# Kernel optimization log

Measured on AMD Instinct MI355X. Metric: run time of the kernel, lower is better.

## Reference

```python
import jax, jax.numpy as jnp
import numpy as np

CANVAS = 28
MARGIN = 2
HALF = CANVAS / 2.0          # 14
SCALE = CANVAS / 2.0 - MARGIN  # 12
P = 2        # num_paths
SEG = 4      # final segments
T = 8        # curve samples per bezier segment
AA = 2       # 2x2 = 4 anti-alias subsamples per pixel


def _lin(x, w, b):
    return x @ w + b


def _render(cp, widths, alphas):
    """diffvg-style rasterizer.
    cp: [B,P,S,4,2] cubic bezier control points, widths/alphas: [B,P].
    Returns [B,1,H,W] image over white background (paths paint dark).
    """
    B = cp.shape[0]
    t = jnp.linspace(0.0, 1.0, T)
    mt = 1.0 - t
    basis = jnp.stack([mt**3, 3*mt**2*t, 3*mt*t**2, t**3], axis=1)  # [T,4]
    pts = jnp.einsum('tk,bpskd->bpstd', basis, cp)                   # [B,P,S,T,2]
    q = pts.reshape(B, P, SEG * T, 2)                                # polyline [B,P,M,2]

    # 2x2 subpixel sample grid over the canvas
    Nf = CANVAS * AA
    c = (jnp.arange(Nf, dtype=jnp.float32) + 0.5) / AA               # fine coords
    sy, sx = jnp.meshgrid(c, c, indexing='ij')
    s = jnp.stack([sx.ravel(), sy.ravel()], axis=-1)                 # [Ns,2] (x,y)

    # stroke coverage: distance from each sample to nearest curve sample
    qq = jnp.sum(q * q, axis=-1)                                     # [B,P,M]
    ss = jnp.sum(s * s, axis=-1)                                     # [Ns]
    cr = jnp.einsum('bpmd,nd->bpmn', q, s)                           # [B,P,M,Ns]
    d2 = jnp.maximum(qq[..., None] + ss - 2.0 * cr, 0.0)
    dist = jnp.sqrt(jnp.min(d2, axis=2))                             # [B,P,Ns]
    stroke = jnp.clip(widths[..., None] * 0.5 + 0.5 - dist, 0.0, 1.0)

    # fill coverage: even-odd crossing number on the closed polyline
    qn = jnp.roll(q, -1, axis=2)
    x0, y0 = q[..., 0], q[..., 1]
    x1, y1 = qn[..., 0], qn[..., 1]
    syf, sxf = s[:, 1], s[:, 0]
    crossing_band = (y0[..., None] > syf) != (y1[..., None] > syf)   # [B,P,M,Ns]
    te = (syf - y0[..., None]) / (y1[..., None] - y0[..., None] + 1e-8)
    xint = x0[..., None] + te * (x1 - x0)[..., None]
    ncross = jnp.sum((crossing_band & (sxf < xint)).astype(jnp.int32), axis=2)
    inside = (ncross % 2).astype(dist.dtype)                         # [B,P,Ns]

    cov = jnp.maximum(inside, stroke)
    img = jnp.prod(1.0 - alphas[..., None] * cov, axis=1)            # composite over paths, bg=1
    img = img.reshape(B, CANVAS, AA, CANVAS, AA).mean(axis=(2, 4))   # AA resolve
    return img[:, None]                                              # [B,1,H,W]


def setup_inputs() -> dict:
    key = jax.random.key(0)
    ks = jax.random.split(key, 16)
    def W(k, i, o):
        return jax.random.normal(k, (i, o), jnp.float32) / np.sqrt(i).astype(np.float32)
    B = 128
    return {
        'x': jax.random.uniform(ks[0], (B, 1, 28, 28), jnp.float32),
        'eps': jax.random.normal(ks[1], (B, 64), jnp.float32),
        'enc_w1': W(ks[2], 784, 256), 'enc_b1': jnp.zeros((256,), jnp.float32),
        'enc_w2': W(ks[3], 256, 256), 'enc_b2': jnp.zeros((256,), jnp.float32),
        'mu_w': W(ks[4], 256, 64), 'mu_b': jnp.zeros((64,), jnp.float32),
        'lv_w': W(ks[5], 256, 64), 'lv_b': jnp.zeros((64,), jnp.float32),
        'dec_w1': W(ks[6], 64, 512), 'dec_b1': jnp.zeros((512,), jnp.float32),
        'dec_w2': W(ks[7], 512, 512), 'dec_b2': jnp.zeros((512,), jnp.float32),
        'cp_w': W(ks[8], 512, 28), 'cp_b': jnp.zeros((28,), jnp.float32),
        'ref_w1': W(ks[9], 92, 512), 'ref_b1': jnp.zeros((512,), jnp.float32),
        'ref_w2': W(ks[10], 512, 52), 'ref_b2': jnp.zeros((52,), jnp.float32),
        'wd_w': W(ks[11], 512, 2), 'wd_b': jnp.zeros((2,), jnp.float32),
        'al_w': W(ks[12], 512, 2), 'al_b': jnp.zeros((2,), jnp.float32),
    }


def reference(x, eps, enc_w1, enc_b1, enc_w2, enc_b2, mu_w, mu_b, lv_w, lv_b,
              dec_w1, dec_b1, dec_w2, dec_b2, cp_w, cp_b,
              ref_w1, ref_b1, ref_w2, ref_b2, wd_w, wd_b, al_w, al_b):
    B = x.shape[0]
    # encoder
    h = jax.nn.leaky_relu(_lin(x.reshape(B, -1), enc_w1, enc_b1), 0.2)
    h = jax.nn.leaky_relu(_lin(h, enc_w2, enc_b2), 0.2)
    mu = _lin(h, mu_w, mu_b)
    logvar = _lin(h, lv_w, lv_b)
    z = mu + eps * jnp.exp(0.5 * logvar)
    # hierarchical decoder
    h2 = jax.nn.selu(_lin(jax.nn.selu(_lin(z, dec_w1, dec_b1)), dec_w2, dec_b2))
    coarse = jnp.tanh(_lin(h2, cp_w, cp_b)).reshape(B, P, 7, 2) * SCALE + HALF
    pts_norm = (coarse - HALF) / SCALE
    h_in = jnp.concatenate([z, pts_norm.reshape(B, -1)], axis=-1)
    refined = jnp.tanh(_lin(jax.nn.selu(_lin(h_in, ref_w1, ref_b1)), ref_w2, ref_b2))
    points = refined.reshape(B, P, 13, 2) * SCALE + HALF
    seg_idx = 3 * jnp.arange(SEG)[:, None] + jnp.arange(4)[None, :]  # [S,4]
    control_points = points[:, :, seg_idx, :]                         # [B,P,S,4,2]
    widths = jax.nn.sigmoid(_lin(h2, wd_w, wd_b)) * 2.0 + 1.0
    alphas = jax.nn.sigmoid(_lin(h2, al_w, al_b))
    rendered = 1.0 - _render(control_points, widths, alphas)          # white digit on black
    return (rendered, mu, logvar, control_points, widths, alphas)
```

## Files before the change

### kernel.cpp

```cpp
#include <hip/hip_runtime.h>
#include <math.h>


#define O_MU  100352
#define O_LV  108544
#define O_CP  116736
#define O_WD  124928
#define O_AL  125184

#define W_H1   0
#define W_HE   32768
#define W_MUT  65536
#define W_LVT  73728
#define W_D1   81920
#define W_H2   147456
#define W_PN   212992
#define W_R1   216576
#define W_PT   282112
#define W_WA   288768

__device__ __forceinline__ float leaky(float x) { return x >= 0.f ? x : 0.2f * x; }
__device__ __forceinline__ float seluf(float x) {
    const float s = 1.0507009873554805f, a = 1.6732632423543772f;
    return x > 0.f ? s * x : s * (a * expm1f(x));
}
__device__ __forceinline__ float sigm(float x) { return 1.f / (1.f + expf(-x)); }

__global__ __launch_bounds__(512)
void enc1_k(const float* __restrict__ x, const float* __restrict__ w,
            const float* __restrict__ b, float* __restrict__ outT) {
    __shared__ float part[8][64];
    const int j = blockIdx.x >> 1, h = blockIdx.x & 1;
    const int tid = threadIdx.x, lane = tid & 63, ks = tid >> 6;
    const int r = h * 64 + lane;
    const float* __restrict__ xr = x + r * 784;
    float acc = 0.f;
    const int k0 = ks * 98;
#pragma unroll 7
    for (int i = 0; i < 98; i++)
        acc = fmaf(xr[k0 + i], w[(k0 + i) * 256 + j], acc);
    part[ks][lane] = acc;
    __syncthreads();
    if (tid < 64) {
        float s = b[j];
#pragma unroll
        for (int q = 0; q < 8; q++) s += part[q][tid];
        outT[j * 128 + h * 64 + tid] = leaky(s);
    }
}

__global__ __launch_bounds__(512)
void enc2_k(const float* __restrict__ inT, const float* __restrict__ w,
            const float* __restrict__ b, float* __restrict__ outT) {
    __shared__ float part[8][64];
    const int j = blockIdx.x >> 1, h = blockIdx.x & 1;
    const int tid = threadIdx.x, lane = tid & 63, ks = tid >> 6;
    const int r = h * 64 + lane;
    float acc = 0.f;
    const int k0 = ks * 32;
#pragma unroll 8
    for (int i = 0; i < 32; i++)
        acc = fmaf(inT[(k0 + i) * 128 + r], w[(k0 + i) * 256 + j], acc);
    part[ks][lane] = acc;
    __syncthreads();
    if (tid < 64) {
        float s = b[j];
#pragma unroll
        for (int q = 0; q < 8; q++) s += part[q][tid];
        outT[j * 128 + h * 64 + tid] = leaky(s);
    }
}

__global__ __launch_bounds__(512)
void mulv_k(const float* __restrict__ heT,
            const float* __restrict__ mu_w, const float* __restrict__ mu_b,
            const float* __restrict__ lv_w, const float* __restrict__ lv_b,
            float* __restrict__ muT, float* __restrict__ lvT,
            float* __restrict__ out) {
    __shared__ float part[8][64];
    const int meta = blockIdx.x >> 1, h = blockIdx.x & 1;
    const int head = meta >> 6, col = meta & 63;
    const float* __restrict__ w = head ? lv_w : mu_w;
    const int tid = threadIdx.x, lane = tid & 63, ks = tid >> 6;
    const int r = h * 64 + lane;
    float acc = 0.f;
    const int k0 = ks * 32;
#pragma unroll 8
    for (int i = 0; i < 32; i++)
        acc = fmaf(heT[(k0 + i) * 128 + r], w[(k0 + i) * 64 + col], acc);
    part[ks][lane] = acc;
    __syncthreads();
    if (tid < 64) {
        float s = (head ? lv_b : mu_b)[col];
#pragma unroll
        for (int q = 0; q < 8; q++) s += part[q][tid];
        const int rr = h * 64 + tid;
        (head ? lvT : muT)[col * 128 + rr] = s;
        out[(head ? O_LV : O_MU) + rr * 64 + col] = s;
    }
}

__global__ __launch_bounds__(512)
void dec1_k(const float* __restrict__ muT, const float* __restrict__ lvT,
            const float* __restrict__ eps, const float* __restrict__ w,
            const float* __restrict__ b, float* __restrict__ outT) {
    __shared__ float part[8][2][64];
    const int j0 = (blockIdx.x >> 1) * 2, h = blockIdx.x & 1;
    const int tid = threadIdx.x, lane = tid & 63, ks = tid >> 6;
    const int r = h * 64 + lane;
    float a0 = 0.f, a1 = 0.f;
    const int k0 = ks * 8;
#pragma unroll
    for (int i = 0; i < 8; i++) {
        const int k = k0 + i;
        float zv = fmaf(eps[r * 64 + k], expf(0.5f * lvT[k * 128 + r]), muT[k * 128 + r]);
        a0 = fmaf(zv, w[k * 512 + j0],     a0);
        a1 = fmaf(zv, w[k * 512 + j0 + 1], a1);
    }
    part[ks][0][lane] = a0; part[ks][1][lane] = a1;
    __syncthreads();
    if (tid < 128) {
        const int c = tid >> 6, ll = tid & 63;
        float s = b[j0 + c];
#pragma unroll
        for (int q = 0; q < 8; q++) s += part[q][c][ll];
        outT[(j0 + c) * 128 + h * 64 + ll] = seluf(s);
    }
}

__global__ __launch_bounds__(512)
void dec2_k(const float* __restrict__ inT, const float* __restrict__ w,
            const float* __restrict__ b, float* __restrict__ outT) {
    __shared__ float part[8][2][64];
    const int j0 = (blockIdx.x >> 1) * 2, h = blockIdx.x & 1;
    const int tid = threadIdx.x, lane = tid & 63, ks = tid >> 6;
    const int r = h * 64 + lane;
    float a0 = 0.f, a1 = 0.f;
    const int k0 = ks * 64;
#pragma unroll 4
    for (int i = 0; i < 64; i++) {
        const float v = inT[(k0 + i) * 128 + r];
        a0 = fmaf(v, w[(k0 + i) * 512 + j0],     a0);
        a1 = fmaf(v, w[(k0 + i) * 512 + j0 + 1], a1);
    }
    part[ks][0][lane] = a0; part[ks][1][lane] = a1;
    __syncthreads();
    if (tid < 128) {
        const int c = tid >> 6, ll = tid & 63;
        float s = b[j0 + c];
#pragma unroll
        for (int q = 0; q < 8; q++) s += part[q][c][ll];
        outT[(j0 + c) * 128 + h * 64 + ll] = seluf(s);
    }
}

__global__ __launch_bounds__(512)
void heads_k(const float* __restrict__ h2T,
             const float* __restrict__ cp_w, const float* __restrict__ cp_b,
             const float* __restrict__ wd_w, const float* __restrict__ wd_b,
             const float* __restrict__ al_w, const float* __restrict__ al_b,
             float* __restrict__ pnT, float* __restrict__ waT,
             float* __restrict__ out) {
    __shared__ float part[8][64];
    const int j = blockIdx.x >> 1, h = blockIdx.x & 1;
    const float* __restrict__ w; int ldw, col;
    if (j < 28)      { w = cp_w; ldw = 28; col = j; }
    else if (j < 30) { w = wd_w; ldw = 2;  col = j - 28; }
    else             { w = al_w; ldw = 2;  col = j - 30; }
    const int tid = threadIdx.x, lane = tid & 63, ks = tid >> 6;
    const int r = h * 64 + lane;
    float acc = 0.f;
    const int k0 = ks * 64;
#pragma unroll 8
    for (int i = 0; i < 64; i++)
        acc = fmaf(h2T[(k0 + i) * 128 + r], w[(k0 + i) * ldw + col], acc);
    part[ks][lane] = acc;
    __syncthreads();
    if (tid < 64) {
        float s = 0.f;
#pragma unroll
        for (int q = 0; q < 8; q++) s += part[q][tid];
        const int rr = h * 64 + tid;
        if (j < 28) {
            pnT[j * 128 + rr] = tanhf(s + cp_b[col]);
        } else if (j < 30) {
            float v = fmaf(sigm(s + wd_b[col]), 2.f, 1.f);
            out[O_WD + rr * 2 + col] = v; waT[col * 128 + rr] = v;
        } else {
            float v = sigm(s + al_b[col]);
            out[O_AL + rr * 2 + col] = v; waT[(2 + col) * 128 + rr] = v;
        }
    }
}

__global__ __launch_bounds__(512)
void ref1_k(const float* __restrict__ muT, const float* __restrict__ lvT,
            const float* __restrict__ eps, const float* __restrict__ pnT,
            const float* __restrict__ w, const float* __restrict__ b,
            float* __restrict__ outT) {
    __shared__ float part[8][2][64];
    const int j0 = (blockIdx.x >> 1) * 2, h = blockIdx.x & 1;
    const int tid = threadIdx.x, lane = tid & 63, ks = tid >> 6;
    const int r = h * 64 + lane;
    float a0 = 0.f, a1 = 0.f;
#pragma unroll
    for (int i = 0; i < 12; i++) {
        const int k = ks * 12 + i;
        if (k < 92) {
            float v = (k < 64)
                ? fmaf(eps[r * 64 + k], expf(0.5f * lvT[k * 128 + r]), muT[k * 128 + r])
                : pnT[(k - 64) * 128 + r];
            a0 = fmaf(v, w[k * 512 + j0],     a0);
            a1 = fmaf(v, w[k * 512 + j0 + 1], a1);
        }
    }
    part[ks][0][lane] = a0; part[ks][1][lane] = a1;
    __syncthreads();
    if (tid < 128) {
        const int c = tid >> 6, ll = tid & 63;
        float s = b[j0 + c];
#pragma unroll
        for (int q = 0; q < 8; q++) s += part[q][c][ll];
        outT[(j0 + c) * 128 + h * 64 + ll] = seluf(s);
    }
}

__global__ __launch_bounds__(512)
void ref2_k(const float* __restrict__ r1T, const float* __restrict__ w,
            const float* __restrict__ b, float* __restrict__ PT) {
    __shared__ float part[8][64];
    const int j = blockIdx.x >> 1, h = blockIdx.x & 1;
    const int tid = threadIdx.x, lane = tid & 63, ks = tid >> 6;
    const int r = h * 64 + lane;
    float acc = 0.f;
    const int k0 = ks * 64;
#pragma unroll 8
    for (int i = 0; i < 64; i++)
        acc = fmaf(r1T[(k0 + i) * 128 + r], w[(k0 + i) * 52 + j], acc);
    part[ks][lane] = acc;
    __syncthreads();
    if (tid < 64) {
        float s = b[j];
#pragma unroll
        for (int q = 0; q < 8; q++) s += part[q][tid];
        PT[j * 128 + h * 64 + tid] = fmaf(tanhf(s), 12.f, 14.f);
    }
}

__global__ __launch_bounds__(512)
void raster_k(const float* __restrict__ PT, const float* __restrict__ waT,
              float* __restrict__ out) {
    __shared__ float sP[56];
    __shared__ float sWA[4];
    __shared__ float sQ[128];
    const int bid = blockIdx.x;
    const int row = bid / 7, chunk = bid - row * 7;
    const int tid = threadIdx.x;
    if (tid < 52) sP[tid] = PT[tid * 128 + row];
    if (tid >= 64 && tid < 68) sWA[tid - 64] = waT[(tid - 64) * 128 + row];
    __syncthreads();
    if (chunk == 0 && tid < 64) {
        const int idx = tid, p = idx >> 5, rest = idx & 31;
        const int s = rest >> 3, kk = (rest >> 1) & 3, d = idx & 1;
        out[O_CP + row * 64 + idx] = sP[p * 26 + (3 * s + kk) * 2 + d];
    }
    if (tid < 128) {
        const int idx = tid, p = idx >> 6, s = (idx >> 4) & 3, ti = (idx >> 1) & 7, d = idx & 1;
        const float t = (float)ti / 7.0f, mt = 1.0f - t;
        const float c0 = mt * mt * mt, c1 = 3.f * mt * mt * t;
        const float c2 = 3.f * mt * t * t, c3 = t * t * t;
        const float* base = sP + p * 26 + 6 * s + d;
        sQ[idx] = c0 * base[0] + c1 * base[2] + c2 * base[4] + c3 * base[6];
    }
    __syncthreads();
    if (tid < 448) {
        const int pixel = chunk * 112 + (tid >> 2), sub = tid & 3;
        const int py = pixel / 28, px = pixel - py * 28;
        const float sy = ((float)(2 * py + (sub >> 1)) + 0.5f) * 0.5f;
        const float sx = ((float)(2 * px + (sub & 1)) + 0.5f) * 0.5f;
        const float2* __restrict__ sQ2 = (const float2*)sQ;
        float img = 1.0f;
#pragma unroll
        for (int p = 0; p < 2; p++) {
            float dmin2 = 1e30f;
            int cnt = 0;
            float2 cur = sQ2[p * 32];
            bool bp = cur.y > sy;
#pragma unroll
            for (int m = 0; m < 32; m++) {
                float2 nxt = sQ2[p * 32 + ((m + 1) & 31)];
                float dx = sx - cur.x;
                float dy = sy - cur.y;
                dmin2 = fminf(dmin2, fmaf(dx, dx, dy * dy));
                bool bn = nxt.y > sy;
                float den = nxt.y - cur.y + 1e-8f;
                float lhs = dx * den;
                float rhs = dy * (nxt.x - cur.x);
                if ((bp != bn) && ((lhs < rhs) == (den > 0.0f))) cnt++;
                cur = nxt;
                bp = bn;
            }
            float dist = sqrtf(dmin2);
            float stroke = fminf(fmaxf(fmaf(sWA[p], 0.5f, 0.5f) - dist, 0.f), 1.f);
            float cov = fmaxf((float)(cnt & 1), stroke);
            img *= fmaf(-sWA[2 + p], cov, 1.0f);
        }
        img += __shfl_xor(img, 1);
        img += __shfl_xor(img, 2);
        if (sub == 0) out[row * 784 + pixel] = 1.0f - 0.25f * img;
    }
}

extern "C" void kernel_launch(void* const* d_in, const int* in_sizes, int n_in,
                              void* d_out, int out_size, void* d_ws, size_t ws_size,
                              hipStream_t stream) {
    const float* x      = (const float*)d_in[0];
    const float* eps    = (const float*)d_in[1];
    const float* enc_w1 = (const float*)d_in[2];
    const float* enc_b1 = (const float*)d_in[3];
    const float* enc_w2 = (const float*)d_in[4];
    const float* enc_b2 = (const float*)d_in[5];
    const float* mu_w   = (const float*)d_in[6];
    const float* mu_b   = (const float*)d_in[7];
    const float* lv_w   = (const float*)d_in[8];
    const float* lv_b   = (const float*)d_in[9];
    const float* dec_w1 = (const float*)d_in[10];
    const float* dec_b1 = (const float*)d_in[11];
    const float* dec_w2 = (const float*)d_in[12];
    const float* dec_b2 = (const float*)d_in[13];
    const float* cp_w   = (const float*)d_in[14];
    const float* cp_b   = (const float*)d_in[15];
    const float* ref_w1 = (const float*)d_in[16];
    const float* ref_b1 = (const float*)d_in[17];
    const float* ref_w2 = (const float*)d_in[18];
    const float* ref_b2 = (const float*)d_in[19];
    const float* wd_w   = (const float*)d_in[20];
    const float* wd_b   = (const float*)d_in[21];
    const float* al_w   = (const float*)d_in[22];
    const float* al_b   = (const float*)d_in[23];

    float* out = (float*)d_out;
    float* ws  = (float*)d_ws;

    enc1_k <<<512, 512, 0, stream>>>(x, enc_w1, enc_b1, ws + W_H1);
    enc2_k <<<512, 512, 0, stream>>>(ws + W_H1, enc_w2, enc_b2, ws + W_HE);
    mulv_k <<<256, 512, 0, stream>>>(ws + W_HE, mu_w, mu_b, lv_w, lv_b,
                                     ws + W_MUT, ws + W_LVT, out);
    dec1_k <<<512, 512, 0, stream>>>(ws + W_MUT, ws + W_LVT, eps,
                                     dec_w1, dec_b1, ws + W_D1);
    dec2_k <<<512, 512, 0, stream>>>(ws + W_D1, dec_w2, dec_b2, ws + W_H2);
    heads_k<<<64, 512, 0, stream>>>(ws + W_H2, cp_w, cp_b, wd_w, wd_b, al_w, al_b,
                                    ws + W_PN, ws + W_WA, out);
    ref1_k <<<512, 512, 0, stream>>>(ws + W_MUT, ws + W_LVT, eps, ws + W_PN,
                                     ref_w1, ref_b1, ws + W_R1);
    ref2_k <<<104, 512, 0, stream>>>(ws + W_R1, ref_w2, ref_b2, ws + W_PT);
    raster_k<<<896, 512, 0, stream>>>(ws + W_PT, ws + W_WA, out);
}
```

Measured before the change: 190.0 us.

## Fuse all nine stages into one persistent kernel with grid barriers

Replaces nine separate kernel launches with a single persistent kernel of 256 blocks. Stages are separated by atomic-counter grid barriers in a zeroed workspace. Blocks loop over work items where the old grids were larger. This removes per-launch overhead and inter-kernel gaps, but adds a memset launch and relies on all 256 blocks being co-resident. The spin barrier has a timeout that could break silently, and its relaxed atomics plus a compiler-only fence may not guarantee cross-block memory visibility.

```diff
diff --git a/kernel.cpp b/kernel.cpp
--- a/kernel.cpp
+++ b/kernel.cpp
@@ -18,6 +18,8 @@
 #define W_R1   216576
 #define W_PT   282112
 #define W_WA   288768
+#define W_BAR  289280
+#define NBLK   256
 
 __device__ __forceinline__ float leaky(float x) { return x >= 0.f ? x : 0.2f * x; }
 __device__ __forceinline__ float seluf(float x) {
@@ -26,288 +28,315 @@
 }
 __device__ __forceinline__ float sigm(float x) { return 1.f / (1.f + expf(-x)); }
 
+__device__ __forceinline__ void stws(float* p, float v) {
+    __hip_atomic_store(p, v, __ATOMIC_RELAXED, __HIP_MEMORY_SCOPE_AGENT);
+}
+
+__device__ __forceinline__ void arrive_wait(unsigned* c) {
+    __syncthreads();
+    if (threadIdx.x == 0) {
+        __hip_atomic_fetch_add(c, 1u, __ATOMIC_RELAXED, __HIP_MEMORY_SCOPE_AGENT);
+        unsigned tries = 0;
+        while (__hip_atomic_load(c, __ATOMIC_RELAXED, __HIP_MEMORY_SCOPE_AGENT) < NBLK) {
+            __builtin_amdgcn_s_sleep(4);
+            if (++tries > (1u << 16)) break;
+        }
+    }
+    __syncthreads();
+    asm volatile("" ::: "memory");
+}
+
 __global__ __launch_bounds__(512)
-void enc1_k(const float* __restrict__ x, const float* __restrict__ w,
-            const float* __restrict__ b, float* __restrict__ outT) {
-    __shared__ float part[8][64];
-    const int j = blockIdx.x >> 1, h = blockIdx.x & 1;
-    const int tid = threadIdx.x, lane = tid & 63, ks = tid >> 6;
-    const int r = h * 64 + lane;
-    const float* __restrict__ xr = x + r * 784;
-    float acc = 0.f;
-    const int k0 = ks * 98;
-#pragma unroll 7
-    for (int i = 0; i < 98; i++)
-        acc = fmaf(xr[k0 + i], w[(k0 + i) * 256 + j], acc);
-    part[ks][lane] = acc;
-    __syncthreads();
-    if (tid < 64) {
-        float s = b[j];
-#pragma unroll
-        for (int q = 0; q < 8; q++) s += part[q][tid];
-        outT[j * 128 + h * 64 + tid] = leaky(s);
-    }
-}
-
-__global__ __launch_bounds__(512)
-void enc2_k(const float* __restrict__ inT, const float* __restrict__ w,
-            const float* __restrict__ b, float* __restrict__ outT) {
-    __shared__ float part[8][64];
-    const int j = blockIdx.x >> 1, h = blockIdx.x & 1;
-    const int tid = threadIdx.x, lane = tid & 63, ks = tid >> 6;
-    const int r = h * 64 + lane;
-    float acc = 0.f;
-    const int k0 = ks * 32;
-#pragma unroll 8
-    for (int i = 0; i < 32; i++)
-        acc = fmaf(inT[(k0 + i) * 128 + r], w[(k0 + i) * 256 + j], acc);
-    part[ks][lane] = acc;
-    __syncthreads();
-    if (tid < 64) {
-        float s = b[j];
-#pragma unroll
-        for (int q = 0; q < 8; q++) s += part[q][tid];
-        outT[j * 128 + h * 64 + tid] = leaky(s);
-    }
-}
-
-__global__ __launch_bounds__(512)
-void mulv_k(const float* __restrict__ heT,
-            const float* __restrict__ mu_w, const float* __restrict__ mu_b,
-            const float* __restrict__ lv_w, const float* __restrict__ lv_b,
-            float* __restrict__ muT, float* __restrict__ lvT,
-            float* __restrict__ out) {
-    __shared__ float part[8][64];
-    const int meta = blockIdx.x >> 1, h = blockIdx.x & 1;
-    const int head = meta >> 6, col = meta & 63;
-    const float* __restrict__ w = head ? lv_w : mu_w;
-    const int tid = threadIdx.x, lane = tid & 63, ks = tid >> 6;
-    const int r = h * 64 + lane;
-    float acc = 0.f;
-    const int k0 = ks * 32;
-#pragma unroll 8
-    for (int i = 0; i < 32; i++)
-        acc = fmaf(heT[(k0 + i) * 128 + r], w[(k0 + i) * 64 + col], acc);
-    part[ks][lane] = acc;
-    __syncthreads();
-    if (tid < 64) {
-        float s = (head ? lv_b : mu_b)[col];
-#pragma unroll
-        for (int q = 0; q < 8; q++) s += part[q][tid];
-        const int rr = h * 64 + tid;
-        (head ? lvT : muT)[col * 128 + rr] = s;
-        out[(head ? O_LV : O_MU) + rr * 64 + col] = s;
-    }
-}
-
-__global__ __launch_bounds__(512)
-void dec1_k(const float* __restrict__ muT, const float* __restrict__ lvT,
-            const float* __restrict__ eps, const float* __restrict__ w,
-            const float* __restrict__ b, float* __restrict__ outT) {
-    __shared__ float part[8][2][64];
-    const int j0 = (blockIdx.x >> 1) * 2, h = blockIdx.x & 1;
-    const int tid = threadIdx.x, lane = tid & 63, ks = tid >> 6;
-    const int r = h * 64 + lane;
-    float a0 = 0.f, a1 = 0.f;
-    const int k0 = ks * 8;
-#pragma unroll
-    for (int i = 0; i < 8; i++) {
-        const int k = k0 + i;
-        float zv = fmaf(eps[r * 64 + k], expf(0.5f * lvT[k * 128 + r]), muT[k * 128 + r]);
-        a0 = fmaf(zv, w[k * 512 + j0],     a0);
-        a1 = fmaf(zv, w[k * 512 + j0 + 1], a1);
-    }
-    part[ks][0][lane] = a0; part[ks][1][lane] = a1;
-    __syncthreads();
-    if (tid < 128) {
-        const int c = tid >> 6, ll = tid & 63;
-        float s = b[j0 + c];
-#pragma unroll
-        for (int q = 0; q < 8; q++) s += part[q][c][ll];
-        outT[(j0 + c) * 128 + h * 64 + ll] = seluf(s);
-    }
-}
-
-__global__ __launch_bounds__(512)
-void dec2_k(const float* __restrict__ inT, const float* __restrict__ w,
-            const float* __restrict__ b, float* __restrict__ outT) {
-    __shared__ float part[8][2][64];
-    const int j0 = (blockIdx.x >> 1) * 2, h = blockIdx.x & 1;
-    const int tid = threadIdx.x, lane = tid & 63, ks = tid >> 6;
-    const int r = h * 64 + lane;
-    float a0 = 0.f, a1 = 0.f;
-    const int k0 = ks * 64;
-#pragma unroll 4
-    for (int i = 0; i < 64; i++) {
-        const float v = inT[(k0 + i) * 128 + r];
-        a0 = fmaf(v, w[(k0 + i) * 512 + j0],     a0);
-        a1 = fmaf(v, w[(k0 + i) * 512 + j0 + 1], a1);
-    }
-    part[ks][0][lane] = a0; part[ks][1][lane] = a1;
-    __syncthreads();
-    if (tid < 128) {
-        const int c = tid >> 6, ll = tid & 63;
-        float s = b[j0 + c];
-#pragma unroll
-        for (int q = 0; q < 8; q++) s += part[q][c][ll];
-        outT[(j0 + c) * 128 + h * 64 + ll] = seluf(s);
-    }
-}
-
-__global__ __launch_bounds__(512)
-void heads_k(const float* __restrict__ h2T,
-             const float* __restrict__ cp_w, const float* __restrict__ cp_b,
-             const float* __restrict__ wd_w, const float* __restrict__ wd_b,
-             const float* __restrict__ al_w, const float* __restrict__ al_b,
-             float* __restrict__ pnT, float* __restrict__ waT,
-             float* __restrict__ out) {
-    __shared__ float part[8][64];
-    const int j = blockIdx.x >> 1, h = blockIdx.x & 1;
-    const float* __restrict__ w; int ldw, col;
-    if (j < 28)      { w = cp_w; ldw = 28; col = j; }
-    else if (j < 30) { w = wd_w; ldw = 2;  col = j - 28; }
-    else             { w = al_w; ldw = 2;  col = j - 30; }
-    const int tid = threadIdx.x, lane = tid & 63, ks = tid >> 6;
-    const int r = h * 64 + lane;
-    float acc = 0.f;
-    const int k0 = ks * 64;
-#pragma unroll 8
-    for (int i = 0; i < 64; i++)
-        acc = fmaf(h2T[(k0 + i) * 128 + r], w[(k0 + i) * ldw + col], acc);
-    part[ks][lane] = acc;
-    __syncthreads();
-    if (tid < 64) {
-        float s = 0.f;
-#pragma unroll
-        for (int q = 0; q < 8; q++) s += part[q][tid];
-        const int rr = h * 64 + tid;
-        if (j < 28) {
-            pnT[j * 128 + rr] = tanhf(s + cp_b[col]);
-        } else if (j < 30) {
-            float v = fmaf(sigm(s + wd_b[col]), 2.f, 1.f);
-            out[O_WD + rr * 2 + col] = v; waT[col * 128 + rr] = v;
-        } else {
-            float v = sigm(s + al_b[col]);
-            out[O_AL + rr * 2 + col] = v; waT[(2 + col) * 128 + rr] = v;
-        }
-    }
-}
-
-__global__ __launch_bounds__(512)
-void ref1_k(const float* __restrict__ muT, const float* __restrict__ lvT,
-            const float* __restrict__ eps, const float* __restrict__ pnT,
-            const float* __restrict__ w, const float* __restrict__ b,
-            float* __restrict__ outT) {
-    __shared__ float part[8][2][64];
-    const int j0 = (blockIdx.x >> 1) * 2, h = blockIdx.x & 1;
-    const int tid = threadIdx.x, lane = tid & 63, ks = tid >> 6;
-    const int r = h * 64 + lane;
-    float a0 = 0.f, a1 = 0.f;
-#pragma unroll
-    for (int i = 0; i < 12; i++) {
-        const int k = ks * 12 + i;
-        if (k < 92) {
-            float v = (k < 64)
-                ? fmaf(eps[r * 64 + k], expf(0.5f * lvT[k * 128 + r]), muT[k * 128 + r])
-                : pnT[(k - 64) * 128 + r];
-            a0 = fmaf(v, w[k * 512 + j0],     a0);
-            a1 = fmaf(v, w[k * 512 + j0 + 1], a1);
-        }
-    }
-    part[ks][0][lane] = a0; part[ks][1][lane] = a1;
-    __syncthreads();
-    if (tid < 128) {
-        const int c = tid >> 6, ll = tid & 63;
-        float s = b[j0 + c];
-#pragma unroll
-        for (int q = 0; q < 8; q++) s += part[q][c][ll];
-        outT[(j0 + c) * 128 + h * 64 + ll] = seluf(s);
-    }
-}
-
-__global__ __launch_bounds__(512)
-void ref2_k(const float* __restrict__ r1T, const float* __restrict__ w,
-            const float* __restrict__ b, float* __restrict__ PT) {
-    __shared__ float part[8][64];
-    const int j = blockIdx.x >> 1, h = blockIdx.x & 1;
-    const int tid = threadIdx.x, lane = tid & 63, ks = tid >> 6;
-    const int r = h * 64 + lane;
-    float acc = 0.f;
-    const int k0 = ks * 64;
-#pragma unroll 8
-    for (int i = 0; i < 64; i++)
-        acc = fmaf(r1T[(k0 + i) * 128 + r], w[(k0 + i) * 52 + j], acc);
-    part[ks][lane] = acc;
-    __syncthreads();
-    if (tid < 64) {
-        float s = b[j];
-#pragma unroll
-        for (int q = 0; q < 8; q++) s += part[q][tid];
-        PT[j * 128 + h * 64 + tid] = fmaf(tanhf(s), 12.f, 14.f);
-    }
-}
-
-__global__ __launch_bounds__(512)
-void raster_k(const float* __restrict__ PT, const float* __restrict__ waT,
-              float* __restrict__ out) {
+void vae_flow(const float* __restrict__ x, const float* __restrict__ eps,
+              const float* __restrict__ enc_w1, const float* __restrict__ enc_b1,
+              const float* __restrict__ enc_w2, const float* __restrict__ enc_b2,
+              const float* __restrict__ mu_w, const float* __restrict__ mu_b,
+              const float* __restrict__ lv_w, const float* __restrict__ lv_b,
+              const float* __restrict__ dec_w1, const float* __restrict__ dec_b1,
+              const float* __restrict__ dec_w2, const float* __restrict__ dec_b2,
+              const float* __restrict__ cp_w, const float* __restrict__ cp_b,
+              const float* __restrict__ ref_w1, const float* __restrict__ ref_b1,
+              const float* __restrict__ ref_w2, const float* __restrict__ ref_b2,
+              const float* __restrict__ wd_w, const float* __restrict__ wd_b,
+              const float* __restrict__ al_w, const float* __restrict__ al_b,
+              float* __restrict__ out, float* __restrict__ ws) {
+    __shared__ float sPart[1024];
     __shared__ float sP[56];
     __shared__ float sWA[4];
     __shared__ float sQ[128];
-    const int bid = blockIdx.x;
-    const int row = bid / 7, chunk = bid - row * 7;
+
+    const int b = blockIdx.x;
     const int tid = threadIdx.x;
-    if (tid < 52) sP[tid] = PT[tid * 128 + row];
-    if (tid >= 64 && tid < 68) sWA[tid - 64] = waT[(tid - 64) * 128 + row];
-    __syncthreads();
-    if (chunk == 0 && tid < 64) {
-        const int idx = tid, p = idx >> 5, rest = idx & 31;
-        const int s = rest >> 3, kk = (rest >> 1) & 3, d = idx & 1;
-        out[O_CP + row * 64 + idx] = sP[p * 26 + (3 * s + kk) * 2 + d];
-    }
-    if (tid < 128) {
-        const int idx = tid, p = idx >> 6, s = (idx >> 4) & 3, ti = (idx >> 1) & 7, d = idx & 1;
-        const float t = (float)ti / 7.0f, mt = 1.0f - t;
-        const float c0 = mt * mt * mt, c1 = 3.f * mt * mt * t;
-        const float c2 = 3.f * mt * t * t, c3 = t * t * t;
-        const float* base = sP + p * 26 + 6 * s + d;
-        sQ[idx] = c0 * base[0] + c1 * base[2] + c2 * base[4] + c3 * base[6];
-    }
-    __syncthreads();
-    if (tid < 448) {
-        const int pixel = chunk * 112 + (tid >> 2), sub = tid & 3;
-        const int py = pixel / 28, px = pixel - py * 28;
-        const float sy = ((float)(2 * py + (sub >> 1)) + 0.5f) * 0.5f;
-        const float sx = ((float)(2 * px + (sub & 1)) + 0.5f) * 0.5f;
+    const int lane = tid & 63, ks = tid >> 6;
+
+    float* const h1T = ws + W_H1;
+    float* const heT = ws + W_HE;
+    float* const muT = ws + W_MUT;
+    float* const lvT = ws + W_LVT;
+    float* const d1T = ws + W_D1;
+    float* const h2T = ws + W_H2;
+    float* const pnT = ws + W_PN;
+    float* const r1T = ws + W_R1;
+    float* const PT  = ws + W_PT;
+    float* const waT = ws + W_WA;
+    unsigned* const bar = (unsigned*)(ws + W_BAR);
+
+    for (int cc = 0; cc < 2; ++cc) {
+        const int c = b + cc * 256;
+        const int j = c >> 1, h = c & 1;
+        const int r = h * 64 + lane;
+        const float* __restrict__ xr = x + r * 784;
+        const int k0 = ks * 98;
+        float acc = 0.f;
+#pragma unroll 7
+        for (int i = 0; i < 98; i++)
+            acc = fmaf(xr[k0 + i], enc_w1[(k0 + i) * 256 + j], acc);
+        sPart[ks * 64 + lane] = acc;
+        __syncthreads();
+        if (tid < 64) {
+            float s = enc_b1[j];
+#pragma unroll
+            for (int q = 0; q < 8; q++) s += sPart[q * 64 + tid];
+            stws(h1T + j * 128 + h * 64 + tid, leaky(s));
+        }
+        __syncthreads();
+    }
+    arrive_wait(bar + 0);
+
+    for (int cc = 0; cc < 2; ++cc) {
+        const int c = b + cc * 256;
+        const int j = c >> 1, h = c & 1;
+        const int r = h * 64 + lane;
+        const int k0 = ks * 32;
+        float acc = 0.f;
+#pragma unroll 8
+        for (int i = 0; i < 32; i++)
+            acc = fmaf(h1T[(k0 + i) * 128 + r], enc_w2[(k0 + i) * 256 + j], acc);
+        sPart[ks * 64 + lane] = acc;
+        __syncthreads();
+        if (tid < 64) {
+            float s = enc_b2[j];
+#pragma unroll
+            for (int q = 0; q < 8; q++) s += sPart[q * 64 + tid];
+            stws(heT + j * 128 + h * 64 + tid, leaky(s));
+        }
+        __syncthreads();
+    }
+    arrive_wait(bar + 1);
+
+    {
+        const int meta = b >> 1, h = b & 1;
+        const int head = meta >> 6, col = meta & 63;
+        const float* __restrict__ w = head ? lv_w : mu_w;
+        const int r = h * 64 + lane;
+        const int k0 = ks * 32;
+        float acc = 0.f;
+#pragma unroll 8
+        for (int i = 0; i < 32; i++)
+            acc = fmaf(heT[(k0 + i) * 128 + r], w[(k0 + i) * 64 + col], acc);
+        sPart[ks * 64 + lane] = acc;
+        __syncthreads();
+        if (tid < 64) {
+            float s = (head ? lv_b : mu_b)[col];
+#pragma unroll
+            for (int q = 0; q < 8; q++) s += sPart[q * 64 + tid];
+            const int rr = h * 64 + tid;
+            stws((head ? lvT : muT) + col * 128 + rr, s);
+            out[(head ? O_LV : O_MU) + rr * 64 + col] = s;
+        }
+        __syncthreads();
+    }
+    arrive_wait(bar + 2);
+
+    for (int cc = 0; cc < 2; ++cc) {
+        const int c = b + cc * 256;
+        const int j0 = (c >> 1) * 2, h = c & 1;
+        const int r = h * 64 + lane;
+        const int k0 = ks * 8;
+        float a0 = 0.f, a1 = 0.f;
+#pragma unroll
+        for (int i = 0; i < 8; i++) {
+            const int k = k0 + i;
+            float zv = fmaf(eps[r * 64 + k], expf(0.5f * lvT[k * 128 + r]), muT[k * 128 + r]);
+            a0 = fmaf(zv, dec_w1[k * 512 + j0],     a0);
+            a1 = fmaf(zv, dec_w1[k * 512 + j0 + 1], a1);
+        }
+        sPart[ks * 128 + lane] = a0; sPart[ks * 128 + 64 + lane] = a1;
+        __syncthreads();
+        if (tid < 128) {
+            const int ci = tid >> 6, ll = tid & 63;
+            float s = dec_b1[j0 + ci];
+#pragma unroll
+            for (int q = 0; q < 8; q++) s += sPart[q * 128 + ci * 64 + ll];
+            stws(d1T + (j0 + ci) * 128 + h * 64 + ll, seluf(s));
+        }
+        __syncthreads();
+    }
+    arrive_wait(bar + 3);
+
+    for (int cc = 0; cc < 2; ++cc) {
+        const int c = b + cc * 256;
+        const int j0 = (c >> 1) * 2, h = c & 1;
+        const int r = h * 64 + lane;
+        const int k0 = ks * 64;
+        float a0 = 0.f, a1 = 0.f;
+#pragma unroll 4
+        for (int i = 0; i < 64; i++) {
+            const float v = d1T[(k0 + i) * 128 + r];
+            a0 = fmaf(v, dec_w2[(k0 + i) * 512 + j0],     a0);
+            a1 = fmaf(v, dec_w2[(k0 + i) * 512 + j0 + 1], a1);
+        }
+        sPart[ks * 128 + lane] = a0; sPart[ks * 128 + 64 + lane] = a1;
+        __syncthreads();
+        if (tid < 128) {
+            const int ci = tid >> 6, ll = tid & 63;
+            float s = dec_b2[j0 + ci];
+#pragma unroll
+            for (int q = 0; q < 8; q++) s += sPart[q * 128 + ci * 64 + ll];
+            stws(h2T + (j0 + ci) * 128 + h * 64 + ll, seluf(s));
+        }
+        __syncthreads();
+    }
+    arrive_wait(bar + 4);
+
+    if (b < 64) {
+        const int j = b >> 1, h = b & 1;
+        const float* __restrict__ w; int ldw, col;
+        if (j < 28)      { w = cp_w; ldw = 28; col = j; }
+        else if (j < 30) { w = wd_w; ldw = 2;  col = j - 28; }
+        else             { w = al_w; ldw = 2;  col = j - 30; }
+        const int r = h * 64 + lane;
+        const int k0 = ks * 64;
+        float acc = 0.f;
+#pragma unroll 8
+        for (int i = 0; i < 64; i++)
+            acc = fmaf(h2T[(k0 + i) * 128 + r], w[(k0 + i) * ldw + col], acc);
+        sPart[ks * 64 + lane] = acc;
+        __syncthreads();
+        if (tid < 64) {
+            float s = 0.f;
+#pragma unroll
+            for (int q = 0; q < 8; q++) s += sPart[q * 64 + tid];
+            const int rr = h * 64 + tid;
+            if (j < 28) {
+                stws(pnT + j * 128 + rr, tanhf(s + cp_b[col]));
+            } else if (j < 30) {
+                float v = fmaf(sigm(s + wd_b[col]), 2.f, 1.f);
+                out[O_WD + rr * 2 + col] = v; stws(waT + col * 128 + rr, v);
+            } else {
+                float v = sigm(s + al_b[col]);
+                out[O_AL + rr * 2 + col] = v; stws(waT + (2 + col) * 128 + rr, v);
+            }
+        }
+        __syncthreads();
+    }
+    arrive_wait(bar + 5);
+
+    for (int cc = 0; cc < 2; ++cc) {
+        const int c = b + cc * 256;
+        const int j0 = (c >> 1) * 2, h = c & 1;
+        const int r = h * 64 + lane;
+        float a0 = 0.f, a1 = 0.f;
+#pragma unroll
+        for (int i = 0; i < 12; i++) {
+            const int k = ks * 12 + i;
+            if (k < 92) {
+                float v = (k < 64)
+                    ? fmaf(eps[r * 64 + k], expf(0.5f * lvT[k * 128 + r]), muT[k * 128 + r])
+                    : pnT[(k - 64) * 128 + r];
+                a0 = fmaf(v, ref_w1[k * 512 + j0],     a0);
+                a1 = fmaf(v, ref_w1[k * 512 + j0 + 1], a1);
+            }
+        }
+        sPart[ks * 128 + lane] = a0; sPart[ks * 128 + 64 + lane] = a1;
+        __syncthreads();
+        if (tid < 128) {
+            const int ci = tid >> 6, ll = tid & 63;
+            float s = ref_b1[j0 + ci];
+#pragma unroll
+            for (int q = 0; q < 8; q++) s += sPart[q * 128 + ci * 64 + ll];
+            stws(r1T + (j0 + ci) * 128 + h * 64 + ll, seluf(s));
+        }
+        __syncthreads();
+    }
+    arrive_wait(bar + 6);
+
+    if (b < 104) {
+        const int j = b >> 1, h = b & 1;
+        const int r = h * 64 + lane;
+        const int k0 = ks * 64;
+        float acc = 0.f;
+#pragma unroll 8
+        for (int i = 0; i < 64; i++)
+            acc = fmaf(r1T[(k0 + i) * 128 + r], ref_w2[(k0 + i) * 52 + j], acc);
+        sPart[ks * 64 + lane] = acc;
+        __syncthreads();
+        if (tid < 64) {
+            float s = ref_b2[j];
+#pragma unroll
+            for (int q = 0; q < 8; q++) s += sPart[q * 64 + tid];
+            stws(PT + j * 128 + h * 64 + tid, fmaf(tanhf(s), 12.f, 14.f));
+        }
+        __syncthreads();
+    }
+    arrive_wait(bar + 7);
+
+    {
+        const int row = b >> 1, half = b & 1;
+        if (tid < 52) sP[tid] = PT[tid * 128 + row];
+        if (tid >= 64 && tid < 68) sWA[tid - 64] = waT[(tid - 64) * 128 + row];
+        __syncthreads();
+        if (half == 0 && tid < 64) {
+            const int idx = tid, p = idx >> 5, rest = idx & 31;
+            const int s = rest >> 3, kk = (rest >> 1) & 3, d = idx & 1;
+            out[O_CP + row * 64 + idx] = sP[p * 26 + (3 * s + kk) * 2 + d];
+        }
+        if (tid < 128) {
+            const int idx = tid, p = idx >> 6, s = (idx >> 4) & 3, ti = (idx >> 1) & 7, d = idx & 1;
+            const float t = (float)ti / 7.0f, mt = 1.0f - t;
+            const float c0 = mt * mt * mt, c1 = 3.f * mt * mt * t;
+            const float c2 = 3.f * mt * t * t, c3 = t * t * t;
+            const float* base = sP + p * 26 + 6 * s + d;
+            sQ[idx] = c0 * base[0] + c1 * base[2] + c2 * base[4] + c3 * base[6];
+        }
+        __syncthreads();
         const float2* __restrict__ sQ2 = (const float2*)sQ;
-        float img = 1.0f;
-#pragma unroll
-        for (int p = 0; p < 2; p++) {
-            float dmin2 = 1e30f;
-            int cnt = 0;
-            float2 cur = sQ2[p * 32];
-            bool bp = cur.y > sy;
-#pragma unroll
-            for (int m = 0; m < 32; m++) {
-                float2 nxt = sQ2[p * 32 + ((m + 1) & 31)];
-                float dx = sx - cur.x;
-                float dy = sy - cur.y;
-                dmin2 = fminf(dmin2, fmaf(dx, dx, dy * dy));
-                bool bn = nxt.y > sy;
-                float den = nxt.y - cur.y + 1e-8f;
-                float lhs = dx * den;
-                float rhs = dy * (nxt.x - cur.x);
-                if ((bp != bn) && ((lhs < rhs) == (den > 0.0f))) cnt++;
-                cur = nxt;
-                bp = bn;
+        for (int u = tid; u < 1568; u += 512) {
+            const int pixel = half * 392 + (u >> 2);
+            const int sub = u & 3;
+            const int py = pixel / 28, px = pixel - py * 28;
+            const float sy = ((float)(2 * py + (sub >> 1)) + 0.5f) * 0.5f;
+            const float sx = ((float)(2 * px + (sub & 1)) + 0.5f) * 0.5f;
+            float img = 1.0f;
+#pragma unroll
+            for (int p = 0; p < 2; p++) {
+                float dmin2 = 1e30f;
+                int cnt = 0;
+                float2 cur = sQ2[p * 32];
+                bool bp = cur.y > sy;
+#pragma unroll
+                for (int m = 0; m < 32; m++) {
+                    float2 nxt = sQ2[p * 32 + ((m + 1) & 31)];
+                    float dx = sx - cur.x;
+                    float dy = sy - cur.y;
+                    dmin2 = fminf(dmin2, fmaf(dx, dx, dy * dy));
+                    bool bn = nxt.y > sy;
+                    float den = nxt.y - cur.y + 1e-8f;
+                    float lhs = dx * den;
+                    float rhs = dy * (nxt.x - cur.x);
+                    if ((bp != bn) && ((lhs < rhs) == (den > 0.0f))) cnt++;
+                    cur = nxt;
+                    bp = bn;
+                }
+                float dist = sqrtf(dmin2);
+                float stroke = fminf(fmaxf(fmaf(sWA[p], 0.5f, 0.5f) - dist, 0.f), 1.f);
+                float cov = fmaxf((float)(cnt & 1), stroke);
+                img *= fmaf(-sWA[2 + p], cov, 1.0f);
             }
-            float dist = sqrtf(dmin2);
-            float stroke = fminf(fmaxf(fmaf(sWA[p], 0.5f, 0.5f) - dist, 0.f), 1.f);
-            float cov = fmaxf((float)(cnt & 1), stroke);
-            img *= fmaf(-sWA[2 + p], cov, 1.0f);
-        }
-        img += __shfl_xor(img, 1);
-        img += __shfl_xor(img, 2);
-        if (sub == 0) out[row * 784 + pixel] = 1.0f - 0.25f * img;
+            img += __shfl_xor(img, 1);
+            img += __shfl_xor(img, 2);
+            if (sub == 0) out[row * 784 + pixel] = 1.0f - 0.25f * img;
+        }
     }
 }
 
@@ -342,17 +371,11 @@
     float* out = (float*)d_out;
     float* ws  = (float*)d_ws;
 
-    enc1_k <<<512, 512, 0, stream>>>(x, enc_w1, enc_b1, ws + W_H1);
-    enc2_k <<<512, 512, 0, stream>>>(ws + W_H1, enc_w2, enc_b2, ws + W_HE);
-    mulv_k <<<256, 512, 0, stream>>>(ws + W_HE, mu_w, mu_b, lv_w, lv_b,
-                                     ws + W_MUT, ws + W_LVT, out);
-    dec1_k <<<512, 512, 0, stream>>>(ws + W_MUT, ws + W_LVT, eps,
-                                     dec_w1, dec_b1, ws + W_D1);
-    dec2_k <<<512, 512, 0, stream>>>(ws + W_D1, dec_w2, dec_b2, ws + W_H2);
-    heads_k<<<64, 512, 0, stream>>>(ws + W_H2, cp_w, cp_b, wd_w, wd_b, al_w, al_b,
-                                    ws + W_PN, ws + W_WA, out);
-    ref1_k <<<512, 512, 0, stream>>>(ws + W_MUT, ws + W_LVT, eps, ws + W_PN,
-                                     ref_w1, ref_b1, ws + W_R1);
-    ref2_k <<<104, 512, 0, stream>>>(ws + W_R1, ref_w2, ref_b2, ws + W_PT);
-    raster_k<<<896, 512, 0, stream>>>(ws + W_PT, ws + W_WA, out);
-}
+    hipMemsetAsync(ws + W_BAR, 0, 8 * sizeof(unsigned), stream);
+
+    vae_flow<<<256, 512, 0, stream>>>(x, eps, enc_w1, enc_b1, enc_w2, enc_b2,
+                                      mu_w, mu_b, lv_w, lv_b, dec_w1, dec_b1,
+                                      dec_w2, dec_b2, cp_w, cp_b, ref_w1, ref_b1,
+                                      ref_w2, ref_b2, wd_w, wd_b, al_w, al_b,
+                                      out, ws);
+}
```

After: 258.1 us. 1.36x slower.
